# Kernel tuning notes

Hardware: AMD Instinct MI355X
Metric: run time of the kernel (lower is better)

## Reference

```python
import jax, jax.numpy as jnp
import numpy as np

N = 50000   # nodes
E = 800000  # edges
F = 128     # feat_dim
LN_EPS = 1e-5


def setup_inputs() -> dict:
    key = jax.random.key(0)
    ks = jax.random.split(key, 16)

    def lin(k, fan_in, shape):
        # roughly kaiming-uniform-like scale; exact init is irrelevant for correctness
        return jax.random.normal(k, shape, jnp.float32) * (1.0 / np.sqrt(fan_in))

    inp = {
        "x": jax.random.normal(ks[0], (N, F), jnp.float32),
        "pos": jax.random.normal(ks[1], (N, 3), jnp.float32),
        "edge_index": jax.random.randint(ks[2], (2, E), 0, N, jnp.int64),
        # edge_mlp: Linear(2F+1 -> F), SiLU, Linear(F -> F)
        "ew1": lin(ks[3], 2 * F + 1, (2 * F + 1, F)),
        "eb1": jnp.zeros((F,), jnp.float32),
        "ew2": lin(ks[4], F, (F, F)),
        "eb2": jnp.zeros((F,), jnp.float32),
        # node_mlp: Linear(F -> F), SiLU, Linear(F -> F)
        "nw1": lin(ks[5], F, (F, F)),
        "nb1": jnp.zeros((F,), jnp.float32),
        "nw2": lin(ks[6], F, (F, F)),
        "nb2": jnp.zeros((F,), jnp.float32),
        # coord_mlp: Linear(F -> 1), Tanh
        "cw": lin(ks[7], F, (F, 1)),
        "cb": jnp.zeros((1,), jnp.float32),
        # LayerNorm(F)
        "gamma": jnp.ones((F,), jnp.float32),
        "beta": jnp.zeros((F,), jnp.float32),
    }
    return inp


def reference(x, pos, edge_index, ew1, eb1, ew2, eb2, nw1, nb1, nw2, nb2, cw, cb, gamma, beta):
    row, col = edge_index[0], edge_index[1]

    diff = pos[row] - pos[col]                              # [E, 3]
    dist2 = jnp.sum(diff * diff, axis=1, keepdims=True)     # [E, 1]
    edge_feat = jnp.concatenate([x[row], x[col], dist2], axis=1)  # [E, 2F+1]

    # edge MLP (dropout p=0 -> identity in eval)
    msg = jax.nn.silu(edge_feat @ ew1 + eb1) @ ew2 + eb2    # [E, F]

    # scatter-add messages to source nodes
    agg = jax.ops.segment_sum(msg, row, num_segments=N)     # [N, F]

    # node MLP + residual + LayerNorm
    upd = jax.nn.silu(agg @ nw1 + nb1) @ nw2 + nb2          # [N, F]
    pre = x + upd
    mean = jnp.mean(pre, axis=-1, keepdims=True)
    var = jnp.mean(jnp.square(pre - mean), axis=-1, keepdims=True)
    x_out = gamma * (pre - mean) * jax.lax.rsqrt(var + LN_EPS) + beta

    # coordinate update
    scale = jnp.tanh(msg @ cw + cb)                         # [E, 1]
    delta = jax.ops.segment_sum(scale * diff, row, num_segments=N)  # [N, 3]
    pos_out = pos + delta
    return (x_out, pos_out)
```

## Files before the change

kernel.cpp:

```cpp
#include <hip/hip_runtime.h>
#include <math.h>

#define NN 50000
#define EE 800000
#define FF 128

constexpr float LN_EPS = 1e-5f;
constexpr int NC = (NN + 255) / 256;

typedef float  f32x4  __attribute__((ext_vector_type(4)));
typedef short  s16x8  __attribute__((ext_vector_type(8)));
typedef unsigned short u16x4 __attribute__((ext_vector_type(4)));

__device__ __forceinline__ float silu_f(float v) {
    return v / (1.f + __expf(-v));
}

__device__ __forceinline__ unsigned short f2bf(float f) {
    union { float f; unsigned u; } cv; cv.f = f;
    unsigned u = cv.u;
    u += 0x7fffu + ((u >> 16) & 1u);
    return (unsigned short)(u >> 16);
}

__device__ __forceinline__ float bf2f(unsigned short u) {
    union { unsigned u; float f; } cv; cv.u = ((unsigned)u) << 16;
    return cv.f;
}

__global__ __launch_bounds__(256) void convert_x_kernel(
    const float* __restrict__ x, unsigned short* __restrict__ xb)
{
    int i = (blockIdx.x * 256 + threadIdx.x) * 8;
    float4 a = *(const float4*)&x[i];
    float4 b = *(const float4*)&x[i + 4];
    s16x8 o;
    o[0] = (short)f2bf(a.x); o[1] = (short)f2bf(a.y);
    o[2] = (short)f2bf(a.z); o[3] = (short)f2bf(a.w);
    o[4] = (short)f2bf(b.x); o[5] = (short)f2bf(b.y);
    o[6] = (short)f2bf(b.z); o[7] = (short)f2bf(b.w);
    *(s16x8*)&xb[i] = o;
}

__global__ __launch_bounds__(256) void transpose_w_kernel(
    const float* __restrict__ ew1, const float* __restrict__ ew2,
    const float* __restrict__ nw1, const float* __restrict__ nw2,
    unsigned short* __restrict__ ew1T, unsigned short* __restrict__ ew2T,
    unsigned short* __restrict__ nw1T, unsigned short* __restrict__ nw2T)
{
    int o = blockIdx.x * 256 + threadIdx.x;
    if (o < 32768) {
        int n = o >> 8, k = o & 255;
        ew1T[o] = f2bf(ew1[k * FF + n]);
    } else if (o < 49152) {
        int o2 = o - 32768; int n = o2 >> 7, k = o2 & 127;
        ew2T[o2] = f2bf(ew2[k * FF + n]);
    } else if (o < 65536) {
        int o2 = o - 49152; int n = o2 >> 7, k = o2 & 127;
        nw1T[o2] = f2bf(nw1[k * FF + n]);
    } else {
        int o2 = o - 65536; int n = o2 >> 7, k = o2 & 127;
        nw2T[o2] = f2bf(nw2[k * FF + n]);
    }
}

__global__ __launch_bounds__(256) void hist_kernel(
    const int* __restrict__ ei, int* __restrict__ cnt)
{
    int e = blockIdx.x * 256 + threadIdx.x;
    if (e < EE) atomicAdd(&cnt[ei[e]], 1);
}

__global__ __launch_bounds__(256) void chunk_sum_kernel(
    const int* __restrict__ cnt, int* __restrict__ chunkSum)
{
    __shared__ int s[256];
    int t = threadIdx.x;
    int idx = blockIdx.x * 256 + t;
    s[t] = (idx < NN) ? cnt[idx] : 0;
    __syncthreads();
    for (int off = 128; off > 0; off >>= 1) {
        if (t < off) s[t] += s[t + off];
        __syncthreads();
    }
    if (t == 0) chunkSum[blockIdx.x] = s[0];
}

__global__ __launch_bounds__(256) void scan_chunks_kernel(
    const int* __restrict__ chunkSum, int* __restrict__ chunkOff)
{
    __shared__ int s[256];
    int t = threadIdx.x;
    int v = (t < NC) ? chunkSum[t] : 0;
    s[t] = v;
    __syncthreads();
    for (int off = 1; off < 256; off <<= 1) {
        int u = (t >= off) ? s[t - off] : 0;
        __syncthreads();
        s[t] += u;
        __syncthreads();
    }
    if (t < NC) chunkOff[t] = s[t] - v;
}

__global__ __launch_bounds__(256) void scan_kernel(
    const int* __restrict__ cnt, const int* __restrict__ chunkOff,
    int* __restrict__ offs, int* __restrict__ rowStart)
{
    __shared__ int s[256];
    int t = threadIdx.x;
    int idx = blockIdx.x * 256 + t;
    int v = (idx < NN) ? cnt[idx] : 0;
    s[t] = v;
    __syncthreads();
    for (int off = 1; off < 256; off <<= 1) {
        int u = (t >= off) ? s[t - off] : 0;
        __syncthreads();
        s[t] += u;
        __syncthreads();
    }
    if (idx < NN) {
        int st = chunkOff[blockIdx.x] + s[t] - v;
        offs[idx] = st;
        rowStart[idx] = st;
    }
}

__global__ __launch_bounds__(256) void scatter_idx_kernel(
    const int* __restrict__ ei, int* __restrict__ offs,
    int* __restrict__ sRow, int* __restrict__ sCol)
{
    int e = blockIdx.x * 256 + threadIdx.x;
    if (e < EE) {
        int r = ei[e], c = ei[EE + e];
        int p = atomicAdd(&offs[r], 1);
        sRow[p] = r;
        sCol[p] = c;
    }
}

constexpr int EPB   = 64;
constexpr int NTILE = EE / EPB;
constexpr int XAS   = 264;
constexpr int H1S   = 136;

__global__ __launch_bounds__(512, 4) void edgeA_kernel(
    const unsigned short* __restrict__ xb, const float* __restrict__ pos,
    const int* __restrict__ sRow, const int* __restrict__ sCol,
    const unsigned short* __restrict__ ew1T, const float* __restrict__ ew1,
    const float* __restrict__ eb1,
    const unsigned short* __restrict__ ew2T, const float* __restrict__ eb2,
    const float* __restrict__ cw,  const float* __restrict__ cb,
    float* __restrict__ agg, float* __restrict__ sSg)
{
    __shared__ float dist2S[EPB];
    __shared__ int   rowS  [EPB];
    __shared__ float sPartT[EPB][8];
    __shared__ __align__(16) unsigned short xa  [EPB * XAS];
    __shared__ __align__(16) unsigned short h1  [EPB * H1S];
    unsigned short* msgL = xa;

    const int t   = threadIdx.x;
    const int w   = t >> 6;
    const int l   = t & 63;
    const int l15 = l & 15;
    const int q8  = l >> 4;
    const int n   = w * 16 + l15;

    s16x8 B1[8], B2[4];
    #pragma unroll
    for (int ko = 0; ko < 8; ++ko)
        B1[ko] = *(const s16x8*)(ew1T + (size_t)n * 256 + ko * 32 + q8 * 8);
    #pragma unroll
    for (int ko = 0; ko < 4; ++ko)
        B2[ko] = *(const s16x8*)(ew2T + (size_t)n * 128 + ko * 32 + q8 * 8);
    const float w256 = ew1[256 * FF + n];
    const float b1   = eb1[n];
    const float b2   = eb2[n];
    const float cwc  = cw[n];
    const float cb0  = cb[0];

    const int q   = t & 31;
    const int eB  = t >> 5;
    const int ksel = (q & 15) * 8;
    const int* idxBase = (q < 16) ? sRow : sCol;

    int   nidx[4];
    s16x8 ag[4];
    {
        int e0 = blockIdx.x * EPB;
        #pragma unroll
        for (int i = 0; i < 4; ++i) nidx[i] = idxBase[e0 + eB + 16 * i];
        #pragma unroll
        for (int i = 0; i < 4; ++i) ag[i] = *(const s16x8*)(xb + (size_t)nidx[i] * FF + ksel);
    }

    for (int tile = blockIdx.x; tile < NTILE; tile += gridDim.x) {
        const int e0 = tile * EPB;

        #pragma unroll
        for (int i = 0; i < 4; ++i)
            *(s16x8*)(xa + (eB + 16 * i) * XAS + q * 8) = ag[i];
        if (t < EPB) {
            int r = sRow[e0 + t];
            int c = sCol[e0 + t];
            rowS[t] = r;
            float dx = pos[r*3+0] - pos[c*3+0];
            float dy = pos[r*3+1] - pos[c*3+1];
            float dz = pos[r*3+2] - pos[c*3+2];
            dist2S[t] = dx*dx + dy*dy + dz*dz;
        }
        __syncthreads();

        {
            int tn  = tile + gridDim.x;
            int e0n = (tn < NTILE) ? tn * EPB : 0;
            #pragma unroll
            for (int i = 0; i < 4; ++i) nidx[i] = idxBase[e0n + eB + 16 * i];
            #pragma unroll
            for (int i = 0; i < 4; ++i) ag[i] = *(const s16x8*)(xb + (size_t)nidx[i] * FF + ksel);
        }

        f32x4 acc[4] = {};
        #pragma unroll
        for (int mt = 0; mt < 4; ++mt) {
            const unsigned short* ar = xa + (mt * 16 + l15) * XAS + q8 * 8;
            #pragma unroll
            for (int ko = 0; ko < 8; ++ko) {
                s16x8 a = *(const s16x8*)(ar + ko * 32);
                acc[mt] = __builtin_amdgcn_mfma_f32_16x16x32_bf16(a, B1[ko], acc[mt], 0, 0, 0);
            }
        }

        #pragma unroll
        for (int mt = 0; mt < 4; ++mt) {
            #pragma unroll
            for (int r = 0; r < 4; ++r) {
                int e = mt * 16 + q8 * 4 + r;
                float v = acc[mt][r] + dist2S[e] * w256 + b1;
                h1[e * H1S + n] = f2bf(silu_f(v));
            }
        }
        __syncthreads();

        f32x4 acc2[4] = {};
        #pragma unroll
        for (int mt = 0; mt < 4; ++mt) {
            const unsigned short* hr = h1 + (mt * 16 + l15) * H1S + q8 * 8;
            #pragma unroll
            for (int ko = 0; ko < 4; ++ko) {
                s16x8 a = *(const s16x8*)(hr + ko * 32);
                acc2[mt] = __builtin_amdgcn_mfma_f32_16x16x32_bf16(a, B2[ko], acc2[mt], 0, 0, 0);
            }
        }

        #pragma unroll
        for (int mt = 0; mt < 4; ++mt) {
            #pragma unroll
            for (int r = 0; r < 4; ++r) {
                float m = acc2[mt][r] + b2;
                float p = m * cwc;
                p += __shfl_xor(p, 1);
                p += __shfl_xor(p, 2);
                p += __shfl_xor(p, 4);
                p += __shfl_xor(p, 8);
                int e = mt * 16 + q8 * 4 + r;
                if (l15 == 0) sPartT[e][w] = p;
                msgL[e * H1S + n] = f2bf(m);
            }
        }
        __syncthreads();

        {
            int e  = t >> 3;
            int ww = t & 7;
            float p = sPartT[e][ww];
            p += __shfl_xor(p, 1);
            p += __shfl_xor(p, 2);
            p += __shfl_xor(p, 4);
            if (ww == 0) sSg[e0 + e] = tanhf(p + cb0);
        }

        {
            int c    = t & 127;
            int s    = t >> 7;
            int base = s * 16;
            float a  = 0.f;
            int cur  = rowS[base];
            #pragma unroll
            for (int k = 0; k < 16; ++k) {
                int e = base + k;
                int r = rowS[e];
                if (r != cur) {
                    atomicAdd(&agg[(size_t)cur * FF + c], a);
                    a = 0.f; cur = r;
                }
                a += bf2f(msgL[e * H1S + c]);
            }
            atomicAdd(&agg[(size_t)cur * FF + c], a);
        }
        __syncthreads();
    }
}

constexpr int NPB = 16;
constexpr int ABS = 136;

__global__ __launch_bounds__(512) void nodeB_kernel(
    const float* __restrict__ x, const float* __restrict__ pos,
    const float* __restrict__ agg, const float* __restrict__ sSg,
    const int* __restrict__ sCol, const int* __restrict__ rowStart,
    const unsigned short* __restrict__ nw1T, const float* __restrict__ nb1,
    const unsigned short* __restrict__ nw2T, const float* __restrict__ nb2,
    const float* __restrict__ gamma, const float* __restrict__ beta,
    float* __restrict__ xout, float* __restrict__ posout)
{
    __shared__ __align__(16) unsigned short aB [NPB * ABS];
    __shared__ __align__(16) unsigned short h1B[NPB * ABS];
    __shared__ float sRedS[8][NPB];
    __shared__ float sRedQ[8][NPB];

    const int t   = threadIdx.x;
    const int w   = t >> 6;
    const int l   = t & 63;
    const int l15 = l & 15;
    const int q8  = l >> 4;
    const int n0  = blockIdx.x * NPB;
    const int n   = w * 16 + l15;

    {
        int idx = t * 4;
        int e = idx >> 7, c = idx & 127;
        float4 v = *(const float4*)&agg[(size_t)(n0 + e) * FF + c];
        u16x4 o;
        o[0] = f2bf(v.x); o[1] = f2bf(v.y); o[2] = f2bf(v.z); o[3] = f2bf(v.w);
        *(u16x4*)(aB + e * ABS + c) = o;
    }

    {
        int e  = t >> 5;
        int ch = t & 31;
        int nn = n0 + e;
        int p0 = rowStart[nn];
        int p1 = (nn == NN - 1) ? EE : rowStart[nn + 1];
        float px = pos[nn*3+0], py = pos[nn*3+1], pz = pos[nn*3+2];
        float sx = 0.f, sy = 0.f, sz = 0.f;
        for (int p = p0 + ch; p < p1; p += 32) {
            int c = sCol[p];
            float g = sSg[p];
            sx += g * (px - pos[c*3+0]);
            sy += g * (py - pos[c*3+1]);
            sz += g * (pz - pos[c*3+2]);
        }
        #pragma unroll
        for (int off = 1; off < 32; off <<= 1) {
            sx += __shfl_xor(sx, off);
            sy += __shfl_xor(sy, off);
            sz += __shfl_xor(sz, off);
        }
        if (ch == 0) {
            posout[nn*3+0] = px + sx;
            posout[nn*3+1] = py + sy;
            posout[nn*3+2] = pz + sz;
        }
    }
    __syncthreads();

    f32x4 acc = {};
    {
        const unsigned short* ar = aB + l15 * ABS + q8 * 8;
        #pragma unroll
        for (int ko = 0; ko < 4; ++ko) {
            s16x8 a = *(const s16x8*)(ar + ko * 32);
            s16x8 b = *(const s16x8*)(nw1T + (size_t)n * 128 + ko * 32 + q8 * 8);
            acc = __builtin_amdgcn_mfma_f32_16x16x32_bf16(a, b, acc, 0, 0, 0);
        }
    }
    {
        float bb = nb1[n];
        #pragma unroll
        for (int r = 0; r < 4; ++r) {
            int e = q8 * 4 + r;
            h1B[e * ABS + n] = f2bf(silu_f(acc[r] + bb));
        }
    }
    __syncthreads();

    f32x4 acc2 = {};
    {
        const unsigned short* hr = h1B + l15 * ABS + q8 * 8;
        #pragma unroll
        for (int ko = 0; ko < 4; ++ko) {
            s16x8 a = *(const s16x8*)(hr + ko * 32);
            s16x8 b = *(const s16x8*)(nw2T + (size_t)n * 128 + ko * 32 + q8 * 8);
            acc2 = __builtin_amdgcn_mfma_f32_16x16x32_bf16(a, b, acc2, 0, 0, 0);
        }
    }

    float pre[4];
    {
        float bb = nb2[n];
        #pragma unroll
        for (int r = 0; r < 4; ++r) {
            int e = q8 * 4 + r;
            pre[r] = x[(size_t)(n0 + e) * FF + n] + acc2[r] + bb;
        }
    }
    #pragma unroll
    for (int r = 0; r < 4; ++r) {
        float s = pre[r], sq = pre[r] * pre[r];
        s += __shfl_xor(s, 1);  sq += __shfl_xor(sq, 1);
        s += __shfl_xor(s, 2);  sq += __shfl_xor(sq, 2);
        s += __shfl_xor(s, 4);  sq += __shfl_xor(sq, 4);
        s += __shfl_xor(s, 8);  sq += __shfl_xor(sq, 8);
        if (l15 == 0) {
            int e = q8 * 4 + r;
            sRedS[w][e] = s;
            sRedQ[w][e] = sq;
        }
    }
    __syncthreads();

    {
        float g = gamma[n], bt = beta[n];
        #pragma unroll
        for (int r = 0; r < 4; ++r) {
            int e = q8 * 4 + r;
            float S = 0.f, Q = 0.f;
            #pragma unroll
            for (int ww = 0; ww < 8; ++ww) { S += sRedS[ww][e]; Q += sRedQ[ww][e]; }
            float mean = S * (1.f / FF);
            float var  = Q * (1.f / FF) - mean * mean;
            xout[(size_t)(n0 + e) * FF + n] =
                g * (pre[r] - mean) * rsqrtf(var + LN_EPS) + bt;
        }
    }
}

extern "C" void kernel_launch(void* const* d_in, const int* in_sizes, int n_in,
                              void* d_out, int out_size, void* d_ws, size_t ws_size,
                              hipStream_t stream) {
    const float* x    = (const float*)d_in[0];
    const float* pos  = (const float*)d_in[1];
    const int*   ei   = (const int*)  d_in[2];
    const float* ew1  = (const float*)d_in[3];
    const float* eb1  = (const float*)d_in[4];
    const float* ew2  = (const float*)d_in[5];
    const float* eb2  = (const float*)d_in[6];
    const float* nw1  = (const float*)d_in[7];
    const float* nb1  = (const float*)d_in[8];
    const float* nw2  = (const float*)d_in[9];
    const float* nb2  = (const float*)d_in[10];
    const float* cw   = (const float*)d_in[11];
    const float* cb   = (const float*)d_in[12];
    const float* gam  = (const float*)d_in[13];
    const float* bet  = (const float*)d_in[14];

    float* out    = (float*)d_out;
    float* xout   = out;
    float* posout = out + (size_t)NN * FF;

    auto align256 = [](size_t v) { return (v + 255) & ~(size_t)255; };
    char* ws = (char*)d_ws;

    size_t CNT_B   = align256((size_t)NN * 4);
    size_t OFFS_B  = align256((size_t)NN * 4);
    size_t RST_B   = align256((size_t)NN * 4);
    size_t CHNK_B  = align256((size_t)NC * 4 * 2);
    size_t SROW_B  = align256((size_t)EE * 4);
    size_t XB_B    = align256((size_t)NN * FF * 2);
    size_t EW1T_B  = align256((size_t)128 * 256 * 2);
    size_t WT_B    = align256((size_t)128 * 128 * 2);
    size_t AGG_B   = align256((size_t)NN * FF * 4);

    size_t o = 0;
    int* cnt       = (int*)(ws + o);  o += CNT_B;
    int* offs      = (int*)(ws + o);  o += OFFS_B;
    int* rowStart  = (int*)(ws + o);  o += RST_B;
    int* chunkSum  = (int*)(ws + o);
    int* chunkOff  = chunkSum + NC;   o += CHNK_B;
    int* sRow      = (int*)(ws + o);  o += SROW_B;
    int* sCol      = (int*)(ws + o);  o += SROW_B;
    unsigned short* xb   = (unsigned short*)(ws + o);  o += XB_B;
    unsigned short* ew1T = (unsigned short*)(ws + o);  o += EW1T_B;
    unsigned short* ew2T = (unsigned short*)(ws + o);  o += WT_B;
    unsigned short* nw1T = (unsigned short*)(ws + o);  o += WT_B;
    unsigned short* nw2T = (unsigned short*)(ws + o);  o += WT_B;
    float*          agg  = (float*)(ws + o);           o += AGG_B;
    float*          sSg  = (float*)(ws + o);

    hipMemsetAsync(cnt, 0, CNT_B, stream);
    hipMemsetAsync(agg, 0, (size_t)NN * FF * 4, stream);

    convert_x_kernel<<<(NN * FF / 8) / 256, 256, 0, stream>>>(x, xb);
    transpose_w_kernel<<<(32768 + 3 * 16384) / 256, 256, 0, stream>>>(
        ew1, ew2, nw1, nw2, ew1T, ew2T, nw1T, nw2T);

    hist_kernel<<<(EE + 255) / 256, 256, 0, stream>>>(ei, cnt);
    chunk_sum_kernel<<<NC, 256, 0, stream>>>(cnt, chunkSum);
    scan_chunks_kernel<<<1, 256, 0, stream>>>(chunkSum, chunkOff);
    scan_kernel<<<NC, 256, 0, stream>>>(cnt, chunkOff, offs, rowStart);
    scatter_idx_kernel<<<(EE + 255) / 256, 256, 0, stream>>>(ei, offs, sRow, sCol);

    edgeA_kernel<<<2048, 512, 0, stream>>>(
        xb, pos, sRow, sCol, ew1T, ew1, eb1, ew2T, eb2, cw, cb, agg, sSg);

    nodeB_kernel<<<NN / NPB, 512, 0, stream>>>(
        x, pos, agg, sSg, sCol, rowStart,
        nw1T, nb1, nw2T, nb2, gam, bet, xout, posout);
}
```

Measured before the change: 514.2 us.

## Remove msg staging and sync in edge kernel, swizzle grid, batch 64 nodes per block

The edge kernel now accumulates messages directly from MFMA accumulators into per-column atomic segment sums, with rows read from a double-buffered rowS. This drops the message staging buffer in shared memory and one barrier per tile. The coordinate-gate partial dot products are atomically added into a raw buffer, and tanh plus bias is applied later in the node kernel, which needs an extra memset. It also adds an XCD-aware block swizzle with a fixed grid of 2500, and grows the node kernel to 64 nodes per block with bounds checks. Risks are many more global atomics, since each of the 8 waves now issues per-edge gate atomics and per-column agg atomics, and possible races on the double-buffered shared arrays without a trailing barrier.

```diff
diff --git a/kernel.cpp b/kernel.cpp
--- a/kernel.cpp
+++ b/kernel.cpp
@@ -139,10 +139,11 @@
     }
 }
 
-constexpr int EPB   = 64;
-constexpr int NTILE = EE / EPB;
-constexpr int XAS   = 264;
-constexpr int H1S   = 136;
+constexpr int EPB    = 64;
+constexpr int NTILE  = EE / EPB;
+constexpr int GRID_A = 2500;
+constexpr int XAS    = 264;
+constexpr int H1S    = 136;
 
 __global__ __launch_bounds__(512, 4) void edgeA_kernel(
     const unsigned short* __restrict__ xb, const float* __restrict__ pos,
@@ -150,15 +151,13 @@
     const unsigned short* __restrict__ ew1T, const float* __restrict__ ew1,
     const float* __restrict__ eb1,
     const unsigned short* __restrict__ ew2T, const float* __restrict__ eb2,
-    const float* __restrict__ cw,  const float* __restrict__ cb,
-    float* __restrict__ agg, float* __restrict__ sSg)
+    const float* __restrict__ cw,
+    float* __restrict__ agg, float* __restrict__ sSgRaw)
 {
     __shared__ float dist2S[EPB];
-    __shared__ int   rowS  [EPB];
-    __shared__ float sPartT[EPB][8];
-    __shared__ __align__(16) unsigned short xa  [EPB * XAS];
-    __shared__ __align__(16) unsigned short h1  [EPB * H1S];
-    unsigned short* msgL = xa;
+    __shared__ int   rowS[2][EPB];
+    __shared__ __align__(16) unsigned short xa[EPB * XAS];
+    __shared__ __align__(16) unsigned short h1[EPB * H1S];
 
     const int t   = threadIdx.x;
     const int w   = t >> 6;
@@ -166,6 +165,13 @@
     const int l15 = l & 15;
     const int q8  = l >> 4;
     const int n   = w * 16 + l15;
+
+    int swz;
+    {
+        const int qd = GRID_A >> 3, r8 = GRID_A & 7;
+        int xcd = blockIdx.x & 7, p8 = blockIdx.x >> 3;
+        swz = (xcd < r8 ? xcd * (qd + 1) : r8 * (qd + 1) + (xcd - r8) * qd) + p8;
+    }
 
     s16x8 B1[8], B2[4];
     #pragma unroll
@@ -178,24 +184,24 @@
     const float b1   = eb1[n];
     const float b2   = eb2[n];
     const float cwc  = cw[n];
-    const float cb0  = cb[0];
-
-    const int q   = t & 31;
-    const int eB  = t >> 5;
+
+    const int q    = t & 31;
+    const int eB   = t >> 5;
     const int ksel = (q & 15) * 8;
     const int* idxBase = (q < 16) ? sRow : sCol;
 
     int   nidx[4];
     s16x8 ag[4];
     {
-        int e0 = blockIdx.x * EPB;
+        int e0 = swz * EPB;
         #pragma unroll
         for (int i = 0; i < 4; ++i) nidx[i] = idxBase[e0 + eB + 16 * i];
         #pragma unroll
         for (int i = 0; i < 4; ++i) ag[i] = *(const s16x8*)(xb + (size_t)nidx[i] * FF + ksel);
     }
 
-    for (int tile = blockIdx.x; tile < NTILE; tile += gridDim.x) {
+    int bsel = 0;
+    for (int tile = swz; tile < NTILE; tile += GRID_A) {
         const int e0 = tile * EPB;
 
         #pragma unroll
@@ -204,7 +210,7 @@
         if (t < EPB) {
             int r = sRow[e0 + t];
             int c = sCol[e0 + t];
-            rowS[t] = r;
+            rowS[bsel][t] = r;
             float dx = pos[r*3+0] - pos[c*3+0];
             float dy = pos[r*3+1] - pos[c*3+1];
             float dz = pos[r*3+2] - pos[c*3+2];
@@ -213,7 +219,7 @@
         __syncthreads();
 
         {
-            int tn  = tile + gridDim.x;
+            int tn  = tile + GRID_A;
             int e0n = (tn < NTILE) ? tn * EPB : 0;
             #pragma unroll
             for (int i = 0; i < 4; ++i) nidx[i] = idxBase[e0n + eB + 16 * i];
@@ -254,65 +260,53 @@
             }
         }
 
-        #pragma unroll
-        for (int mt = 0; mt < 4; ++mt) {
-            #pragma unroll
-            for (int r = 0; r < 4; ++r) {
-                float m = acc2[mt][r] + b2;
-                float p = m * cwc;
-                p += __shfl_xor(p, 1);
-                p += __shfl_xor(p, 2);
-                p += __shfl_xor(p, 4);
-                p += __shfl_xor(p, 8);
-                int e = mt * 16 + q8 * 4 + r;
-                if (l15 == 0) sPartT[e][w] = p;
-                msgL[e * H1S + n] = f2bf(m);
-            }
-        }
-        __syncthreads();
-
         {
-            int e  = t >> 3;
-            int ww = t & 7;
-            float p = sPartT[e][ww];
-            p += __shfl_xor(p, 1);
-            p += __shfl_xor(p, 2);
-            p += __shfl_xor(p, 4);
-            if (ww == 0) sSg[e0 + e] = tanhf(p + cb0);
-        }
-
-        {
-            int c    = t & 127;
-            int s    = t >> 7;
-            int base = s * 16;
+            int4 rws[4];
+            #pragma unroll
+            for (int mt = 0; mt < 4; ++mt)
+                rws[mt] = *(const int4*)&rowS[bsel][mt * 16 + q8 * 4];
+
             float a  = 0.f;
-            int cur  = rowS[base];
-            #pragma unroll
-            for (int k = 0; k < 16; ++k) {
-                int e = base + k;
-                int r = rowS[e];
-                if (r != cur) {
-                    atomicAdd(&agg[(size_t)cur * FF + c], a);
-                    a = 0.f; cur = r;
+            int  cur = rws[0].x;
+            #pragma unroll
+            for (int mt = 0; mt < 4; ++mt) {
+                #pragma unroll
+                for (int r = 0; r < 4; ++r) {
+                    float m = acc2[mt][r] + b2;
+                    float p = m * cwc;
+                    p += __shfl_xor(p, 1);
+                    p += __shfl_xor(p, 2);
+                    p += __shfl_xor(p, 4);
+                    p += __shfl_xor(p, 8);
+                    if (l15 == 0)
+                        atomicAdd(&sSgRaw[e0 + mt * 16 + q8 * 4 + r], p);
+                    int rr = (r == 0) ? rws[mt].x : (r == 1) ? rws[mt].y :
+                             (r == 2) ? rws[mt].z : rws[mt].w;
+                    if (rr != cur) {
+                        atomicAdd(&agg[(size_t)cur * FF + n], a);
+                        a = 0.f; cur = rr;
+                    }
+                    a += m;
                 }
-                a += bf2f(msgL[e * H1S + c]);
-            }
-            atomicAdd(&agg[(size_t)cur * FF + c], a);
-        }
-        __syncthreads();
-    }
-}
-
-constexpr int NPB = 16;
-constexpr int ABS = 136;
+            }
+            atomicAdd(&agg[(size_t)cur * FF + n], a);
+        }
+        bsel ^= 1;
+    }
+}
+
+constexpr int NPB  = 64;
+constexpr int ABS  = 136;
+constexpr int NBLK = (NN + NPB - 1) / NPB;
 
 __global__ __launch_bounds__(512) void nodeB_kernel(
     const float* __restrict__ x, const float* __restrict__ pos,
-    const float* __restrict__ agg, const float* __restrict__ sSg,
+    const float* __restrict__ agg, const float* __restrict__ sSgRaw,
     const int* __restrict__ sCol, const int* __restrict__ rowStart,
     const unsigned short* __restrict__ nw1T, const float* __restrict__ nb1,
     const unsigned short* __restrict__ nw2T, const float* __restrict__ nb2,
     const float* __restrict__ gamma, const float* __restrict__ beta,
+    const float* __restrict__ cb,
     float* __restrict__ xout, float* __restrict__ posout)
 {
     __shared__ __align__(16) unsigned short aB [NPB * ABS];
@@ -327,38 +321,47 @@
     const int q8  = l >> 4;
     const int n0  = blockIdx.x * NPB;
     const int n   = w * 16 + l15;
-
-    {
-        int idx = t * 4;
+    const float cb0 = cb[0];
+
+    #pragma unroll
+    for (int i = 0; i < 4; ++i) {
+        int idx = (i * 512 + t) * 4;
         int e = idx >> 7, c = idx & 127;
-        float4 v = *(const float4*)&agg[(size_t)(n0 + e) * FF + c];
         u16x4 o;
-        o[0] = f2bf(v.x); o[1] = f2bf(v.y); o[2] = f2bf(v.z); o[3] = f2bf(v.w);
+        if (n0 + e < NN) {
+            float4 v = *(const float4*)&agg[(size_t)(n0 + e) * FF + c];
+            o[0] = f2bf(v.x); o[1] = f2bf(v.y); o[2] = f2bf(v.z); o[3] = f2bf(v.w);
+        } else {
+            o[0] = 0; o[1] = 0; o[2] = 0; o[3] = 0;
+        }
         *(u16x4*)(aB + e * ABS + c) = o;
     }
 
     {
-        int e  = t >> 5;
-        int ch = t & 31;
+        int e  = t >> 3;
+        int ch = t & 7;
         int nn = n0 + e;
-        int p0 = rowStart[nn];
-        int p1 = (nn == NN - 1) ? EE : rowStart[nn + 1];
-        float px = pos[nn*3+0], py = pos[nn*3+1], pz = pos[nn*3+2];
+        bool ok = nn < NN;
+        int p0 = ok ? rowStart[nn] : 0;
+        int p1 = ok ? ((nn == NN - 1) ? EE : rowStart[nn + 1]) : 0;
+        float px = ok ? pos[nn*3+0] : 0.f;
+        float py = ok ? pos[nn*3+1] : 0.f;
+        float pz = ok ? pos[nn*3+2] : 0.f;
         float sx = 0.f, sy = 0.f, sz = 0.f;
-        for (int p = p0 + ch; p < p1; p += 32) {
+        for (int p = p0 + ch; p < p1; p += 8) {
             int c = sCol[p];
-            float g = sSg[p];
+            float g = tanhf(sSgRaw[p] + cb0);
             sx += g * (px - pos[c*3+0]);
             sy += g * (py - pos[c*3+1]);
             sz += g * (pz - pos[c*3+2]);
         }
         #pragma unroll
-        for (int off = 1; off < 32; off <<= 1) {
+        for (int off = 1; off < 8; off <<= 1) {
             sx += __shfl_xor(sx, off);
             sy += __shfl_xor(sy, off);
             sz += __shfl_xor(sz, off);
         }
-        if (ch == 0) {
+        if (ch == 0 && ok) {
             posout[nn*3+0] = px + sx;
             posout[nn*3+1] = py + sy;
             posout[nn*3+2] = pz + sz;
@@ -366,73 +369,102 @@
     }
     __syncthreads();
 
-    f32x4 acc = {};
-    {
-        const unsigned short* ar = aB + l15 * ABS + q8 * 8;
-        #pragma unroll
-        for (int ko = 0; ko < 4; ++ko) {
-            s16x8 a = *(const s16x8*)(ar + ko * 32);
-            s16x8 b = *(const s16x8*)(nw1T + (size_t)n * 128 + ko * 32 + q8 * 8);
-            acc = __builtin_amdgcn_mfma_f32_16x16x32_bf16(a, b, acc, 0, 0, 0);
+    f32x4 acc[4] = {};
+    {
+        s16x8 bw[4];
+        #pragma unroll
+        for (int ko = 0; ko < 4; ++ko)
+            bw[ko] = *(const s16x8*)(nw1T + (size_t)n * 128 + ko * 32 + q8 * 8);
+        #pragma unroll
+        for (int mt = 0; mt < 4; ++mt) {
+            const unsigned short* ar = aB + (mt * 16 + l15) * ABS + q8 * 8;
+            #pragma unroll
+            for (int ko = 0; ko < 4; ++ko) {
+                s16x8 a = *(const s16x8*)(ar + ko * 32);
+                acc[mt] = __builtin_amdgcn_mfma_f32_16x16x32_bf16(a, bw[ko], acc[mt], 0, 0, 0);
+            }
         }
     }
     {
         float bb = nb1[n];
         #pragma unroll
+        for (int mt = 0; mt < 4; ++mt) {
+            #pragma unroll
+            for (int r = 0; r < 4; ++r) {
+                int e = mt * 16 + q8 * 4 + r;
+                h1B[e * ABS + n] = f2bf(silu_f(acc[mt][r] + bb));
+            }
+        }
+    }
+    __syncthreads();
+
+    f32x4 acc2[4] = {};
+    {
+        s16x8 bw[4];
+        #pragma unroll
+        for (int ko = 0; ko < 4; ++ko)
+            bw[ko] = *(const s16x8*)(nw2T + (size_t)n * 128 + ko * 32 + q8 * 8);
+        #pragma unroll
+        for (int mt = 0; mt < 4; ++mt) {
+            const unsigned short* hr = h1B + (mt * 16 + l15) * ABS + q8 * 8;
+            #pragma unroll
+            for (int ko = 0; ko < 4; ++ko) {
+                s16x8 a = *(const s16x8*)(hr + ko * 32);
+                acc2[mt] = __builtin_amdgcn_mfma_f32_16x16x32_bf16(a, bw[ko], acc2[mt], 0, 0, 0);
+            }
+        }
+    }
+
+    float pre[4][4];
+    {
+        float bb = nb2[n];
+        #pragma unroll
+        for (int mt = 0; mt < 4; ++mt) {
+            #pragma unroll
+            for (int r = 0; r < 4; ++r) {
+                int e  = mt * 16 + q8 * 4 + r;
+                int nn = n0 + e;
+                float xv = (nn < NN) ? x[(size_t)nn * FF + n] : 0.f;
+                pre[mt][r] = xv + acc2[mt][r] + bb;
+            }
+        }
+    }
+    #pragma unroll
+    for (int mt = 0; mt < 4; ++mt) {
+        #pragma unroll
         for (int r = 0; r < 4; ++r) {
-            int e = q8 * 4 + r;
-            h1B[e * ABS + n] = f2bf(silu_f(acc[r] + bb));
+            float s = pre[mt][r], sq = pre[mt][r] * pre[mt][r];
+            s += __shfl_xor(s, 1);  sq += __shfl_xor(sq, 1);
+            s += __shfl_xor(s, 2);  sq += __shfl_xor(sq, 2);
+            s += __shfl_xor(s, 4);  sq += __shfl_xor(sq, 4);
+            s += __shfl_xor(s, 8);  sq += __shfl_xor(sq, 8);
+            if (l15 == 0) {
+                int e = mt * 16 + q8 * 4 + r;
+                sRedS[w][e] = s;
+                sRedQ[w][e] = sq;
+            }
         }
     }
     __syncthreads();
 
-    f32x4 acc2 = {};
-    {
-        const unsigned short* hr = h1B + l15 * ABS + q8 * 8;
-        #pragma unroll
-        for (int ko = 0; ko < 4; ++ko) {
-            s16x8 a = *(const s16x8*)(hr + ko * 32);
-            s16x8 b = *(const s16x8*)(nw2T + (size_t)n * 128 + ko * 32 + q8 * 8);
-            acc2 = __builtin_amdgcn_mfma_f32_16x16x32_bf16(a, b, acc2, 0, 0, 0);
-        }
-    }
-
-    float pre[4];
-    {
-        float bb = nb2[n];
-        #pragma unroll
-        for (int r = 0; r < 4; ++r) {
-            int e = q8 * 4 + r;
-            pre[r] = x[(size_t)(n0 + e) * FF + n] + acc2[r] + bb;
-        }
-    }
-    #pragma unroll
-    for (int r = 0; r < 4; ++r) {
-        float s = pre[r], sq = pre[r] * pre[r];
-        s += __shfl_xor(s, 1);  sq += __shfl_xor(sq, 1);
-        s += __shfl_xor(s, 2);  sq += __shfl_xor(sq, 2);
-        s += __shfl_xor(s, 4);  sq += __shfl_xor(sq, 4);
-        s += __shfl_xor(s, 8);  sq += __shfl_xor(sq, 8);
-        if (l15 == 0) {
-            int e = q8 * 4 + r;
-            sRedS[w][e] = s;
-            sRedQ[w][e] = sq;
-        }
-    }
-    __syncthreads();
-
     {
         float g = gamma[n], bt = beta[n];
         #pragma unroll
-        for (int r = 0; r < 4; ++r) {
-            int e = q8 * 4 + r;
-            float S = 0.f, Q = 0.f;
-            #pragma unroll
-            for (int ww = 0; ww < 8; ++ww) { S += sRedS[ww][e]; Q += sRedQ[ww][e]; }
-            float mean = S * (1.f / FF);
-            float var  = Q * (1.f / FF) - mean * mean;
-            xout[(size_t)(n0 + e) * FF + n] =
-                g * (pre[r] - mean) * rsqrtf(var + LN_EPS) + bt;
+        for (int mt = 0; mt < 4; ++mt) {
+            #pragma unroll
+            for (int r = 0; r < 4; ++r) {
+                int e  = mt * 16 + q8 * 4 + r;
+                int nn = n0 + e;
+                if (nn < NN) {
+                    float S = 0.f, Q = 0.f;
+                    #pragma unroll
+                    for (int ww = 0; ww < 8; ++ww) { S += sRedS[ww][e]; Q += sRedQ[ww][e]; }
+                    float mean = S * (1.f / FF);
+                    float var  = Q * (1.f / FF) - mean * mean;
+                    xout[(size_t)nn * FF + n] =
+                        g * (pre[mt][r] - mean) * rsqrtf(var + LN_EPS) + bt;
+                }
+            }
         }
     }
 }
@@ -486,11 +518,12 @@
     unsigned short* ew2T = (unsigned short*)(ws + o);  o += WT_B;
     unsigned short* nw1T = (unsigned short*)(ws + o);  o += WT_B;
     unsigned short* nw2T = (unsigned short*)(ws + o);  o += WT_B;
-    float*          agg  = (float*)(ws + o);           o += AGG_B;
-    float*          sSg  = (float*)(ws + o);
+    float*          agg    = (float*)(ws + o);         o += AGG_B;
+    float*          sSgRaw = (float*)(ws + o);
 
     hipMemsetAsync(cnt, 0, CNT_B, stream);
     hipMemsetAsync(agg, 0, (size_t)NN * FF * 4, stream);
+    hipMemsetAsync(sSgRaw, 0, (size_t)EE * 4, stream);
 
     convert_x_kernel<<<(NN * FF / 8) / 256, 256, 0, stream>>>(x, xb);
     transpose_w_kernel<<<(32768 + 3 * 16384) / 256, 256, 0, stream>>>(
@@ -502,10 +535,10 @@
     scan_kernel<<<NC, 256, 0, stream>>>(cnt, chunkOff, offs, rowStart);
     scatter_idx_kernel<<<(EE + 255) / 256, 256, 0, stream>>>(ei, offs, sRow, sCol);
 
-    edgeA_kernel<<<2048, 512, 0, stream>>>(
-        xb, pos, sRow, sCol, ew1T, ew1, eb1, ew2T, eb2, cw, cb, agg, sSg);
-
-    nodeB_kernel<<<NN / NPB, 512, 0, stream>>>(
-        x, pos, agg, sSg, sCol, rowStart,
-        nw1T, nb1, nw2T, nb2, gam, bet, xout, posout);
-}
+    edgeA_kernel<<<GRID_A, 512, 0, stream>>>(
+        xb, pos, sRow, sCol, ew1T, ew1, eb1, ew2T, eb2, cw, agg, sSgRaw);
+
+    nodeB_kernel<<<NBLK, 512, 0, stream>>>(
+        x, pos, agg, sSgRaw, sCol, rowStart,
+        nw1T, nb1, nw2T, nb2, gam, bet, cb, xout, posout);
+}
```

After: 594.9 us. 15.7% more time.
